# Performance work log

Hardware: AMD Instinct MI355X
Metric: run time of the kernel (lower is better)

## Reference

```python
import jax, jax.numpy as jnp
import numpy as np

EPS = 1e-6

def _ln(x, w, b):
    mu = jnp.mean(x, axis=-1, keepdims=True)
    var = jnp.mean((x - mu) ** 2, axis=-1, keepdims=True)
    return (x - mu) * jax.lax.rsqrt(var + EPS) * w + b

def setup_inputs() -> dict:
    B, N, C, H, P = 64, 197, 768, 12, 20
    Dh = C // H
    Dff = 4 * C
    key = jax.random.key(0)
    ks = jax.random.split(key, 16)
    s = 0.02
    return {
        "x": jax.random.normal(ks[0], (B, N, C), jnp.float32),
        "prompt": jax.random.normal(ks[1], (B, P, 2, H, Dh), jnp.float32),
        "ln1_w": jnp.ones((C,), jnp.float32),
        "ln1_b": jnp.zeros((C,), jnp.float32),
        "qkv_w": jax.random.normal(ks[2], (3 * C, C), jnp.float32) * s,
        "qkv_b": jnp.zeros((3 * C,), jnp.float32),
        "proj_w": jax.random.normal(ks[3], (C, C), jnp.float32) * s,
        "proj_b": jnp.zeros((C,), jnp.float32),
        "ln2_w": jnp.ones((C,), jnp.float32),
        "ln2_b": jnp.zeros((C,), jnp.float32),
        "fc1_w": jax.random.normal(ks[4], (Dff, C), jnp.float32) * s,
        "fc1_b": jnp.zeros((Dff,), jnp.float32),
        "fc2_w": jax.random.normal(ks[5], (C, Dff), jnp.float32) * s,
        "fc2_b": jnp.zeros((C,), jnp.float32),
    }

def reference(x, prompt, ln1_w, ln1_b, qkv_w, qkv_b, proj_w, proj_b,
              ln2_w, ln2_b, fc1_w, fc1_b, fc2_w, fc2_b):
    B, N, C = x.shape
    H = 12
    Dh = C // H
    scale = Dh ** -0.5

    # --- attention branch ---
    h = _ln(x, ln1_w, ln1_b)
    qkv = (h @ qkv_w.T + qkv_b).reshape(B, N, 3, H, Dh)
    qkv = jnp.transpose(qkv, (2, 0, 3, 1, 4))  # [3, B, H, N, Dh]
    q, k, v = qkv[0], qkv[1], qkv[2]

    # prompt: [B, P, 2, H, Dh] -> [2, B, H, P, Dh]
    pr = jnp.transpose(prompt, (2, 0, 3, 1, 4))
    k = jnp.concatenate([pr[0], k], axis=2)  # [B, H, P+N, Dh]
    v = jnp.concatenate([pr[1], v], axis=2)

    attn = jnp.einsum('bhnd,bhmd->bhnm', q, k) * scale
    attn = jax.nn.softmax(attn, axis=-1)
    o = jnp.einsum('bhnm,bhmd->bhnd', attn, v)
    o = jnp.transpose(o, (0, 2, 1, 3)).reshape(B, N, C)
    o = o @ proj_w.T + proj_b
    x = x + o

    # --- mlp branch ---
    h2 = _ln(x, ln2_w, ln2_b)
    m = jax.nn.gelu(h2 @ fc1_w.T + fc1_b, approximate=False)
    m = m @ fc2_w.T + fc2_b
    return x + m
```

## Files before the change

### kernel.cpp

```cpp
#include <hip/hip_runtime.h>
#include <hip/hip_bf16.h>

typedef __attribute__((ext_vector_type(4))) float f32x4;
typedef __attribute__((ext_vector_type(8))) __bf16 bfv8;
typedef __attribute__((ext_vector_type(8))) short sv8;
typedef __attribute__((ext_vector_type(4))) unsigned short usv4;


static __device__ __forceinline__ f32x4 mfma16(sv8 a, sv8 b, f32x4 c) {
    return __builtin_amdgcn_mfma_f32_16x16x32_bf16(
        __builtin_bit_cast(bfv8, a), __builtin_bit_cast(bfv8, b), c, 0, 0, 0);
}

static __device__ __forceinline__ unsigned short f2bf(float f) {
    union { float f; unsigned int u; } v; v.f = f;
    unsigned int u = v.u;
    return (unsigned short)((u + 0x7FFFu + ((u >> 16) & 1u)) >> 16);
}

static __device__ __forceinline__ void gld16(void* lds, const void* g) {
    __builtin_amdgcn_global_load_lds(
        (const __attribute__((address_space(1))) unsigned int*)g,
        (__attribute__((address_space(3))) unsigned int*)lds, 16, 0, 0);
}


__global__ void cvt_bf16_kernel(const float* __restrict__ in,
                                unsigned short* __restrict__ out, int n4) {
    int i = blockIdx.x * 256 + threadIdx.x;
    if (i >= n4) return;
    float4 f = reinterpret_cast<const float4*>(in)[i];
    usv4 o = { f2bf(f.x), f2bf(f.y), f2bf(f.z), f2bf(f.w) };
    reinterpret_cast<usv4*>(out)[i] = o;
}


__global__ void ln_kernel(const float* __restrict__ x, const float* __restrict__ w,
                          const float* __restrict__ b, unsigned short* __restrict__ out) {
    const int row = blockIdx.x;
    const int t = threadIdx.x;
    const float* xr = x + (size_t)row * 768;
    float v[3];
    float s = 0.f, ss = 0.f;
#pragma unroll
    for (int i = 0; i < 3; ++i) {
        v[i] = xr[t + i * 256];
        s += v[i]; ss += v[i] * v[i];
    }
#pragma unroll
    for (int o = 32; o; o >>= 1) { s += __shfl_xor(s, o); ss += __shfl_xor(ss, o); }
    __shared__ float red[8];
    if ((t & 63) == 0) { red[t >> 6] = s; red[4 + (t >> 6)] = ss; }
    __syncthreads();
    float S = red[0] + red[1] + red[2] + red[3];
    float SS = red[4] + red[5] + red[6] + red[7];
    float mu = S * (1.0f / 768.0f);
    float var = SS * (1.0f / 768.0f) - mu * mu;
    float rstd = rsqrtf(var + 1e-6f);
#pragma unroll
    for (int i = 0; i < 3; ++i) {
        int c = t + i * 256;
        out[(size_t)row * 768 + c] = f2bf((v[i] - mu) * rstd * w[c] + b[c]);
    }
}


__global__ void prompt_kernel(const float* __restrict__ pr,
                              unsigned short* __restrict__ k_out,
                              unsigned short* __restrict__ v_out) {
    int i = blockIdx.x * 256 + threadIdx.x;
    if (i >= 64 * 20 * 12 * 64) return;
    int d = i & 63;
    int t = i >> 6;
    int h = t % 12;
    int t2 = t / 12;
    int p = t2 % 20;
    int b = t2 / 20;
    size_t src = ((((size_t)b * 20 + p) * 2 + 0) * 12 + h) * 64 + d;
    float kv = pr[src];
    float vv = pr[src + 12 * 64];
    k_out[(((size_t)(b * 12 + h) * 224 + p) << 6) + d] = f2bf(kv);
    v_out[((size_t)(b * 12 + h) * 64 + d) * 224 + p] = f2bf(vv);
}


#define EPI_QKV 0
#define EPI_RES 1
#define EPI_GELU 2

template <int EPI, int WM, int WN>
__global__ void __launch_bounds__(WM * WN * 64)
gemm_bf16(const unsigned short* __restrict__ A,
          const unsigned short* __restrict__ W,
          const float* __restrict__ bias,
          const float* __restrict__ resid,
          void* __restrict__ out0,
          unsigned short* __restrict__ q_out,
          unsigned short* __restrict__ k_out,
          unsigned short* __restrict__ v_out,
          int M, int N, int K, int NB) {
    constexpr int THREADS = WM * WN * 64;
    constexpr int BM = WM * 64, BN = WN * 64;
    constexpr int NCA = (BM * 4) / THREADS;
    constexpr int NCB = (BN * 4) / THREADS;
    __shared__ __align__(16) unsigned short As[2][BM * 32];
    __shared__ __align__(16) unsigned short Bs[2][BN * 32];
    const int tid = threadIdx.x;
    const int lane = tid & 63;
    const int wv = tid >> 6;
    const int wm = wv / WN, wn = wv % WN;
    const int rl = lane & 15, kg = lane >> 4;

    const int nwg = gridDim.x;
    const int orig = blockIdx.x;
    const int xcd = orig & 7;
    const int qq = nwg >> 3, rr = nwg & 7;
    const int wg = (xcd < rr ? xcd * (qq + 1) : rr * (qq + 1) + (xcd - rr) * qq) + (orig >> 3);
    const int bm = wg / NB, bn = wg - bm * NB;

    const unsigned short* pA[NCA];
    const unsigned short* pB[NCB];
#pragma unroll
    for (int i = 0; i < NCA; ++i) {
        const int c = i * THREADS + tid;
        const int row = c >> 2, sl = c & 3;
        int ar = bm * BM + row; ar = ar < M ? ar : M - 1;
        pA[i] = A + (size_t)ar * K + sl * 8;
    }
#pragma unroll
    for (int i = 0; i < NCB; ++i) {
        const int c = i * THREADS + tid;
        const int row = c >> 2, sl = c & 3;
        pB[i] = W + (size_t)(bn * BN + row) * K + sl * 8;
    }
    auto stage = [&](int sb, int kt) {
        const int k0 = kt << 5;
#pragma unroll
        for (int i = 0; i < NCA; ++i)
            gld16(&As[sb][(i * THREADS + tid) * 8], pA[i] + k0);
#pragma unroll
        for (int i = 0; i < NCB; ++i)
            gld16(&Bs[sb][(i * THREADS + tid) * 8], pB[i] + k0);
    };

    f32x4 acc[4][4];
#pragma unroll
    for (int i = 0; i < 4; ++i)
#pragma unroll
        for (int j = 0; j < 4; ++j) acc[i][j] = f32x4{0.f, 0.f, 0.f, 0.f};

    const int nk = K >> 5;
    stage(0, 0);
    __syncthreads();
    for (int kt = 0; kt < nk; ++kt) {
        const int cur = kt & 1;
        if (kt + 1 < nk) stage(cur ^ 1, kt + 1);
        sv8 af[4], bfr[4];
#pragma unroll
        for (int f = 0; f < 4; ++f) {
            const int ra = wm * 64 + f * 16 + rl;
            af[f] = *reinterpret_cast<const sv8*>(&As[cur][ra * 32 + kg * 8]);
            const int rb = wn * 64 + f * 16 + rl;
            bfr[f] = *reinterpret_cast<const sv8*>(&Bs[cur][rb * 32 + kg * 8]);
        }
#pragma unroll
        for (int i = 0; i < 4; ++i)
#pragma unroll
            for (int j = 0; j < 4; ++j) acc[i][j] = mfma16(af[i], bfr[j], acc[i][j]);
        __syncthreads();
    }

#pragma unroll
    for (int i = 0; i < 4; ++i) {
        const int m0 = bm * BM + wm * 64 + i * 16 + kg * 4;
#pragma unroll
        for (int j = 0; j < 4; ++j) {
            const int ncol = bn * BN + wn * 64 + j * 16 + rl;
            const float bia = bias[ncol];
#pragma unroll
            for (int r = 0; r < 4; ++r) {
                const int m = m0 + r;
                if (m >= M) continue;
                float vv = acc[i][j][r] + bia;
                if constexpr (EPI == EPI_QKV) {
                    int b = m / 197, nn = m - b * 197;
                    int which = ncol / 768;
                    int rc = ncol - which * 768;
                    int h = rc >> 6;
                    int d = ncol & 63;
                    if (which == 0)
                        q_out[(((size_t)(b * 12 + h) * 197 + nn) << 6) + d] = f2bf(vv);
                    else if (which == 1)
                        k_out[(((size_t)(b * 12 + h) * 224 + 20 + nn) << 6) + d] = f2bf(vv);
                    else
                        v_out[((size_t)(b * 12 + h) * 64 + d) * 224 + 20 + nn] = f2bf(vv);
                } else if constexpr (EPI == EPI_RES) {
                    ((float*)out0)[(size_t)m * N + ncol] = vv + resid[(size_t)m * N + ncol];
                } else {
                    float g = vv / (1.0f + __expf(-1.5957691216f * vv * (1.0f + 0.044715f * vv * vv)));
                    ((unsigned short*)out0)[(size_t)m * N + ncol] = f2bf(g);
                }
            }
        }
    }
}


__global__ void attn_kernel(const unsigned short* __restrict__ Qg,
                            const unsigned short* __restrict__ Kg,
                            const unsigned short* __restrict__ Vtg,
                            unsigned short* __restrict__ obuf) {
    __shared__ __align__(16) unsigned short sKS[14848];
    __shared__ __align__(16) unsigned short sV[64 * 232];
    const int tid = threadIdx.x;
    const int lane = tid & 63;
    const int wave = tid >> 6;
    const int rl = lane & 15, kg = lane >> 4;
    const int qt = blockIdx.x, h = blockIdx.y, b = blockIdx.z;
    const size_t bh = (size_t)b * 12 + h;
    const size_t qbase = bh * 197 * 64;
    const size_t kbase = bh * 224 * 64;
    const size_t vbase = bh * 64 * 224;

    int qrow = qt * 64 + wave * 16 + rl;
    if (qrow > 196) qrow = 196;
    sv8 qf[2];
#pragma unroll
    for (int ks = 0; ks < 2; ++ks)
        qf[ks] = *reinterpret_cast<const sv8*>(&Qg[qbase + (size_t)qrow * 64 + ks * 32 + kg * 8]);

#pragma unroll
    for (int i = 0; i < 7; ++i) {
        const int c = i * 256 + tid;
        const int key = c >> 3, sl = c & 7;
        const int ssl = sl ^ (key & 7);
        gld16(&sKS[c * 8], &Kg[kbase + key * 64 + ssl * 8]);
    }
#pragma unroll
    for (int i = 0; i < 7; ++i) {
        const int c = i * 256 + tid;
        const int d = c / 28, sl = c - d * 28;
        sv8 val = *reinterpret_cast<const sv8*>(&Vtg[vbase + d * 224 + sl * 8]);
        *reinterpret_cast<sv8*>(&sV[d * 232 + sl * 8]) = val;
    }
    __syncthreads();

    f32x4 sacc[14];
#pragma unroll
    for (int f = 0; f < 14; ++f) sacc[f] = f32x4{0.f, 0.f, 0.f, 0.f};
#pragma unroll
    for (int f = 0; f < 14; ++f) {
        const int key = f * 16 + rl;
#pragma unroll
        for (int ks = 0; ks < 2; ++ks) {
            const int sl = (ks * 4 + kg) ^ (key & 7);
            sv8 kf = *reinterpret_cast<const sv8*>(&sKS[key * 64 + sl * 8]);
            sacc[f] = mfma16(qf[ks], kf, sacc[f]);
        }
    }

    float mx[4] = {-1e30f, -1e30f, -1e30f, -1e30f};
#pragma unroll
    for (int f = 0; f < 14; ++f) {
        const int col = f * 16 + rl;
#pragma unroll
        for (int r = 0; r < 4; ++r) {
            float s = sacc[f][r] * 0.125f;
            if (col >= 217) s = -1e30f;
            sacc[f][r] = s;
            mx[r] = fmaxf(mx[r], s);
        }
    }
#pragma unroll
    for (int o = 1; o < 16; o <<= 1)
#pragma unroll
        for (int r = 0; r < 4; ++r) mx[r] = fmaxf(mx[r], __shfl_xor(mx[r], o));
    float sm[4] = {0.f, 0.f, 0.f, 0.f};
#pragma unroll
    for (int f = 0; f < 14; ++f)
#pragma unroll
        for (int r = 0; r < 4; ++r) {
            float e = __expf(sacc[f][r] - mx[r]);
            sacc[f][r] = e;
            sm[r] += e;
        }
#pragma unroll
    for (int o = 1; o < 16; o <<= 1)
#pragma unroll
        for (int r = 0; r < 4; ++r) sm[r] += __shfl_xor(sm[r], o);
    float inv[4];
#pragma unroll
    for (int r = 0; r < 4; ++r) inv[r] = 1.0f / sm[r];

    __syncthreads();
    unsigned short* Sl = sKS;
#pragma unroll
    for (int f = 0; f < 14; ++f)
#pragma unroll
        for (int r = 0; r < 4; ++r)
            Sl[(wave * 16 + kg * 4 + r) * 232 + f * 16 + rl] = f2bf(sacc[f][r] * inv[r]);
    __syncthreads();

    f32x4 oacc[4];
#pragma unroll
    for (int fd = 0; fd < 4; ++fd) oacc[fd] = f32x4{0.f, 0.f, 0.f, 0.f};
#pragma unroll
    for (int ks = 0; ks < 7; ++ks) {
        sv8 pf = *reinterpret_cast<const sv8*>(&Sl[(wave * 16 + rl) * 232 + ks * 32 + kg * 8]);
#pragma unroll
        for (int fd = 0; fd < 4; ++fd) {
            sv8 vf = *reinterpret_cast<const sv8*>(&sV[(fd * 16 + rl) * 232 + ks * 32 + kg * 8]);
            oacc[fd] = mfma16(pf, vf, oacc[fd]);
        }
    }

#pragma unroll
    for (int fd = 0; fd < 4; ++fd)
#pragma unroll
        for (int r = 0; r < 4; ++r) {
            const int q = qt * 64 + wave * 16 + kg * 4 + r;
            if (q < 197)
                obuf[((size_t)b * 197 + q) * 768 + h * 64 + fd * 16 + rl] = f2bf(oacc[fd][r]);
        }
}


extern "C" void kernel_launch(void* const* d_in, const int* in_sizes, int n_in,
                              void* d_out, int out_size, void* d_ws, size_t ws_size,
                              hipStream_t stream) {
    const float* x      = (const float*)d_in[0];
    const float* prompt = (const float*)d_in[1];
    const float* ln1_w  = (const float*)d_in[2];
    const float* ln1_b  = (const float*)d_in[3];
    const float* qkv_w  = (const float*)d_in[4];
    const float* qkv_b  = (const float*)d_in[5];
    const float* proj_w = (const float*)d_in[6];
    const float* proj_b = (const float*)d_in[7];
    const float* ln2_w  = (const float*)d_in[8];
    const float* ln2_b  = (const float*)d_in[9];
    const float* fc1_w  = (const float*)d_in[10];
    const float* fc1_b  = (const float*)d_in[11];
    const float* fc2_w  = (const float*)d_in[12];
    const float* fc2_b  = (const float*)d_in[13];

    char* ws = (char*)d_ws;
    size_t off = 0;
    auto bump = [&](size_t bytes) {
        char* p = ws + off;
        off += (bytes + 255) & ~(size_t)255;
        return p;
    };
    unsigned short* qkvw  = (unsigned short*)bump(2304UL * 768 * 2);
    unsigned short* projw = (unsigned short*)bump(768UL * 768 * 2);
    unsigned short* fc1w  = (unsigned short*)bump(3072UL * 768 * 2);
    unsigned short* fc2w  = (unsigned short*)bump(768UL * 3072 * 2);
    unsigned short* h2    = (unsigned short*)bump(12608UL * 768 * 2);
    float* xmid           = (float*)bump(12608UL * 768 * 4);
    char* pool = ws + off;
    unsigned short* h1   = (unsigned short*)(pool);
    unsigned short* Qg   = (unsigned short*)(pool + 19365888UL);
    unsigned short* Kg   = (unsigned short*)(pool + 38731776UL);
    unsigned short* Vtg  = (unsigned short*)(pool + 60751872UL);
    unsigned short* obuf = (unsigned short*)(pool + 82771968UL);
    unsigned short* mbuf = (unsigned short*)(pool);

    cvt_bf16_kernel<<<(2304 * 768 / 4 + 255) / 256, 256, 0, stream>>>(qkv_w, qkvw, 2304 * 768 / 4);
    cvt_bf16_kernel<<<(768 * 768 / 4 + 255) / 256, 256, 0, stream>>>(proj_w, projw, 768 * 768 / 4);
    cvt_bf16_kernel<<<(3072 * 768 / 4 + 255) / 256, 256, 0, stream>>>(fc1_w, fc1w, 3072 * 768 / 4);
    cvt_bf16_kernel<<<(768 * 3072 / 4 + 255) / 256, 256, 0, stream>>>(fc2_w, fc2w, 768 * 3072 / 4);

    ln_kernel<<<12608, 256, 0, stream>>>(x, ln1_w, ln1_b, h1);
    prompt_kernel<<<983040 / 256, 256, 0, stream>>>(prompt, Kg, Vtg);

    gemm_bf16<EPI_QKV, 4, 4><<<50 * 9, 1024, 0, stream>>>(
        h1, qkvw, qkv_b, nullptr, nullptr, Qg, Kg, Vtg, 12608, 2304, 768, 9);

    attn_kernel<<<dim3(4, 12, 64), 256, 0, stream>>>(Qg, Kg, Vtg, obuf);

    gemm_bf16<EPI_RES, 2, 2><<<99 * 6, 256, 0, stream>>>(
        obuf, projw, proj_b, x, xmid, nullptr, nullptr, nullptr, 12608, 768, 768, 6);

    ln_kernel<<<12608, 256, 0, stream>>>(xmid, ln2_w, ln2_b, h2);

    gemm_bf16<EPI_GELU, 4, 4><<<50 * 12, 1024, 0, stream>>>(
        h2, fc1w, fc1_b, nullptr, mbuf, nullptr, nullptr, nullptr, 12608, 3072, 768, 12);

    gemm_bf16<EPI_RES, 2, 2><<<99 * 6, 256, 0, stream>>>(
        mbuf, fc2w, fc2_b, xmid, (float*)d_out, nullptr, nullptr, nullptr, 12608, 768, 3072, 6);
}
```

Before: 444.2 us.

## Fuse weight conversion, prompt packing and LN1 into one prep kernel; retile GEMMs

Merges the four weight-conversion launches, the prompt K/V packing kernel and the first LayerNorm into a single block-dispatched prep kernel. LayerNorm now reads and writes float4 vectors using 192 active threads per row. The QKV and FC1 GEMMs move from 256x256 tiles with 1024 threads to 256x128 tiles with 512 threads, doubling the grid. The aim is lower launch overhead and better CU occupancy on the large GEMMs, at the cost of more A-tile reloads.

```diff
diff --git a/kernel.cpp b/kernel.cpp
--- a/kernel.cpp
+++ b/kernel.cpp
@@ -25,157 +25,103 @@
 }
 
 
-__global__ void cvt_bf16_kernel(const float* __restrict__ in,
-                                unsigned short* __restrict__ out, int n4) {
-    int i = blockIdx.x * 256 + threadIdx.x;
-    if (i >= n4) return;
-    float4 f = reinterpret_cast<const float4*>(in)[i];
-    usv4 o = { f2bf(f.x), f2bf(f.y), f2bf(f.z), f2bf(f.w) };
-    reinterpret_cast<usv4*>(out)[i] = o;
-}
-
+static __device__ __forceinline__ void ln_row(const float* __restrict__ xr,
+                                              const float* __restrict__ w,
+                                              const float* __restrict__ b,
+                                              unsigned short* __restrict__ outr,
+                                              int t) {
+    __shared__ float red[8];
+    float4 v = {0.f, 0.f, 0.f, 0.f};
+    float s = 0.f, ss = 0.f;
+    if (t < 192) {
+        v = reinterpret_cast<const float4*>(xr)[t];
+        s = v.x + v.y + v.z + v.w;
+        ss = v.x * v.x + v.y * v.y + v.z * v.z + v.w * v.w;
+    }
+#pragma unroll
+    for (int o = 32; o; o >>= 1) { s += __shfl_xor(s, o); ss += __shfl_xor(ss, o); }
+    if ((t & 63) == 0) { red[t >> 6] = s; red[4 + (t >> 6)] = ss; }
+    __syncthreads();
+    const float S = red[0] + red[1] + red[2];
+    const float SS = red[4] + red[5] + red[6];
+    const float mu = S * (1.0f / 768.0f);
+    const float var = SS * (1.0f / 768.0f) - mu * mu;
+    const float rstd = rsqrtf(var + 1e-6f);
+    if (t < 192) {
+        float4 wv = reinterpret_cast<const float4*>(w)[t];
+        float4 bv = reinterpret_cast<const float4*>(b)[t];
+        usv4 o = { f2bf((v.x - mu) * rstd * wv.x + bv.x),
+                   f2bf((v.y - mu) * rstd * wv.y + bv.y),
+                   f2bf((v.z - mu) * rstd * wv.z + bv.z),
+                   f2bf((v.w - mu) * rstd * wv.w + bv.w) };
+        reinterpret_cast<usv4*>(outr)[t] = o;
+    }
+}
 
 __global__ void ln_kernel(const float* __restrict__ x, const float* __restrict__ w,
                           const float* __restrict__ b, unsigned short* __restrict__ out) {
-    const int row = blockIdx.x;
-    const int t = threadIdx.x;
-    const float* xr = x + (size_t)row * 768;
-    float v[3];
-    float s = 0.f, ss = 0.f;
-#pragma unroll
-    for (int i = 0; i < 3; ++i) {
-        v[i] = xr[t + i * 256];
-        s += v[i]; ss += v[i] * v[i];
-    }
-#pragma unroll
-    for (int o = 32; o; o >>= 1) { s += __shfl_xor(s, o); ss += __shfl_xor(ss, o); }
-    __shared__ float red[8];
-    if ((t & 63) == 0) { red[t >> 6] = s; red[4 + (t >> 6)] = ss; }
-    __syncthreads();
-    float S = red[0] + red[1] + red[2] + red[3];
-    float SS = red[4] + red[5] + red[6] + red[7];
-    float mu = S * (1.0f / 768.0f);
-    float var = SS * (1.0f / 768.0f) - mu * mu;
-    float rstd = rsqrtf(var + 1e-6f);
-#pragma unroll
-    for (int i = 0; i < 3; ++i) {
-        int c = t + i * 256;
-        out[(size_t)row * 768 + c] = f2bf((v[i] - mu) * rstd * w[c] + b[c]);
-    }
-}
-
-
-__global__ void prompt_kernel(const float* __restrict__ pr,
-                              unsigned short* __restrict__ k_out,
-                              unsigned short* __restrict__ v_out) {
-    int i = blockIdx.x * 256 + threadIdx.x;
-    if (i >= 64 * 20 * 12 * 64) return;
-    int d = i & 63;
-    int t = i >> 6;
-    int h = t % 12;
-    int t2 = t / 12;
-    int p = t2 % 20;
-    int b = t2 / 20;
-    size_t src = ((((size_t)b * 20 + p) * 2 + 0) * 12 + h) * 64 + d;
-    float kv = pr[src];
-    float vv = pr[src + 12 * 64];
-    k_out[(((size_t)(b * 12 + h) * 224 + p) << 6) + d] = f2bf(kv);
-    v_out[((size_t)(b * 12 + h) * 64 + d) * 224 + p] = f2bf(vv);
-}
-
+    const size_t row = blockIdx.x;
+    ln_row(x + row * 768, w, b, out + row * 768, threadIdx.x);
+}
+
+
+__global__ void prep_kernel(const float* __restrict__ qkv_w, const float* __restrict__ proj_w,
+                            const float* __restrict__ fc1_w, const float* __restrict__ fc2_w,
+                            unsigned short* __restrict__ qkvw, unsigned short* __restrict__ projw,
+                            unsigned short* __restrict__ fc1w, unsigned short* __restrict__ fc2w,
+                            const float* __restrict__ pr,
+                            unsigned short* __restrict__ k_out, unsigned short* __restrict__ v_out,
+                            const float* __restrict__ x, const float* __restrict__ ln1_w,
+                            const float* __restrict__ ln1_b, unsigned short* __restrict__ h1) {
+    const int blk = blockIdx.x;
+    const int tid = threadIdx.x;
+    if (blk < 6912) {
+        const float* in;
+        unsigned short* out;
+        int i;
+        if (blk < 1728)      { in = qkv_w; out = qkvw; i = blk * 256 + tid; }
+        else if (blk < 2304) { in = proj_w; out = projw; i = (blk - 1728) * 256 + tid; }
+        else if (blk < 4608) { in = fc1_w; out = fc1w; i = (blk - 2304) * 256 + tid; }
+        else                 { in = fc2_w; out = fc2w; i = (blk - 4608) * 256 + tid; }
+        float4 f = reinterpret_cast<const float4*>(in)[i];
+        usv4 o = { f2bf(f.x), f2bf(f.y), f2bf(f.z), f2bf(f.w) };
+        reinterpret_cast<usv4*>(out)[i] = o;
+    } else if (blk < 10752) {
+        const int i = (blk - 6912) * 256 + tid;
+        const int d = i & 63;
+        const int t = i >> 6;
+        const int h = t % 12;
+        const int t2 = t / 12;
+        const int p = t2 % 20;
+        const int b = t2 / 20;
+        size_t src = ((((size_t)b * 20 + p) * 2 + 0) * 12 + h) * 64 + d;
+        float kv = pr[src];
+        float vv = pr[src + 12 * 64];
+        k_out[(((size_t)(b * 12 + h) * 224 + p) << 6) + d] = f2bf(kv);
+        v_out[((size_t)(b * 12 + h) * 64 + d) * 224 + p] = f2bf(vv);
+    } else {
+        const size_t row = blk - 10752;
+        ln_row(x + row * 768, ln1_w, ln1_b, h1 + row * 768, tid);
+    }
+}
 
 #define EPI_QKV 0
 #define EPI_RES 1
 #define EPI_GELU 2
 
-template <int EPI, int WM, int WN>
-__global__ void __launch_bounds__(WM * WN * 64)
-gemm_bf16(const unsigned short* __restrict__ A,
-          const unsigned short* __restrict__ W,
-          const float* __restrict__ bias,
-          const float* __restrict__ resid,
-          void* __restrict__ out0,
-          unsigned short* __restrict__ q_out,
-          unsigned short* __restrict__ k_out,
-          unsigned short* __restrict__ v_out,
-          int M, int N, int K, int NB) {
-    constexpr int THREADS = WM * WN * 64;
-    constexpr int BM = WM * 64, BN = WN * 64;
-    constexpr int NCA = (BM * 4) / THREADS;
-    constexpr int NCB = (BN * 4) / THREADS;
-    __shared__ __align__(16) unsigned short As[2][BM * 32];
-    __shared__ __align__(16) unsigned short Bs[2][BN * 32];
-    const int tid = threadIdx.x;
-    const int lane = tid & 63;
-    const int wv = tid >> 6;
-    const int wm = wv / WN, wn = wv % WN;
-    const int rl = lane & 15, kg = lane >> 4;
-
-    const int nwg = gridDim.x;
-    const int orig = blockIdx.x;
-    const int xcd = orig & 7;
-    const int qq = nwg >> 3, rr = nwg & 7;
-    const int wg = (xcd < rr ? xcd * (qq + 1) : rr * (qq + 1) + (xcd - rr) * qq) + (orig >> 3);
-    const int bm = wg / NB, bn = wg - bm * NB;
-
-    const unsigned short* pA[NCA];
-    const unsigned short* pB[NCB];
-#pragma unroll
-    for (int i = 0; i < NCA; ++i) {
-        const int c = i * THREADS + tid;
-        const int row = c >> 2, sl = c & 3;
-        int ar = bm * BM + row; ar = ar < M ? ar : M - 1;
-        pA[i] = A + (size_t)ar * K + sl * 8;
-    }
-#pragma unroll
-    for (int i = 0; i < NCB; ++i) {
-        const int c = i * THREADS + tid;
-        const int row = c >> 2, sl = c & 3;
-        pB[i] = W + (size_t)(bn * BN + row) * K + sl * 8;
-    }
-    auto stage = [&](int sb, int kt) {
-        const int k0 = kt << 5;
-#pragma unroll
-        for (int i = 0; i < NCA; ++i)
-            gld16(&As[sb][(i * THREADS + tid) * 8], pA[i] + k0);
-#pragma unroll
-        for (int i = 0; i < NCB; ++i)
-            gld16(&Bs[sb][(i * THREADS + tid) * 8], pB[i] + k0);
-    };
-
-    f32x4 acc[4][4];
-#pragma unroll
-    for (int i = 0; i < 4; ++i)
-#pragma unroll
-        for (int j = 0; j < 4; ++j) acc[i][j] = f32x4{0.f, 0.f, 0.f, 0.f};
-
-    const int nk = K >> 5;
-    stage(0, 0);
-    __syncthreads();
-    for (int kt = 0; kt < nk; ++kt) {
-        const int cur = kt & 1;
-        if (kt + 1 < nk) stage(cur ^ 1, kt + 1);
-        sv8 af[4], bfr[4];
-#pragma unroll
-        for (int f = 0; f < 4; ++f) {
-            const int ra = wm * 64 + f * 16 + rl;
-            af[f] = *reinterpret_cast<const sv8*>(&As[cur][ra * 32 + kg * 8]);
-            const int rb = wn * 64 + f * 16 + rl;
-            bfr[f] = *reinterpret_cast<const sv8*>(&Bs[cur][rb * 32 + kg * 8]);
-        }
-#pragma unroll
-        for (int i = 0; i < 4; ++i)
-#pragma unroll
-            for (int j = 0; j < 4; ++j) acc[i][j] = mfma16(af[i], bfr[j], acc[i][j]);
-        __syncthreads();
-    }
-
+
+template <int EPI>
+static __device__ __forceinline__ void gemm_epilogue(
+        f32x4 (&acc)[4][4], int bmBase, int bnBase, int wm, int wn,
+        int rl, int kg, const float* bias, const float* resid, void* out0,
+        unsigned short* q_out, unsigned short* k_out, unsigned short* v_out,
+        int M, int N) {
 #pragma unroll
     for (int i = 0; i < 4; ++i) {
-        const int m0 = bm * BM + wm * 64 + i * 16 + kg * 4;
+        const int m0 = bmBase + wm * 64 + i * 16 + kg * 4;
 #pragma unroll
         for (int j = 0; j < 4; ++j) {
-            const int ncol = bn * BN + wn * 64 + j * 16 + rl;
+            const int ncol = bnBase + wn * 64 + j * 16 + rl;
             const float bia = bias[ncol];
 #pragma unroll
             for (int r = 0; r < 4; ++r) {
@@ -206,6 +152,92 @@
 }
 
 
+template <int EPI, int WM, int WN>
+__global__ void __launch_bounds__(WM * WN * 64)
+gemm_bf16(const unsigned short* __restrict__ A,
+          const unsigned short* __restrict__ W,
+          const float* __restrict__ bias,
+          const float* __restrict__ resid,
+          void* __restrict__ out0,
+          unsigned short* __restrict__ q_out,
+          unsigned short* __restrict__ k_out,
+          unsigned short* __restrict__ v_out,
+          int M, int N, int K, int NB) {
+    constexpr int THREADS = WM * WN * 64;
+    constexpr int BM = WM * 64, BN = WN * 64;
+    constexpr int NCA = (BM * 4) / THREADS;
+    constexpr int NCB = (BN * 4) / THREADS;
+    __shared__ __align__(16) unsigned short As[2][BM * 32];
+    __shared__ __align__(16) unsigned short Bs[2][BN * 32];
+    const int tid = threadIdx.x;
+    const int lane = tid & 63;
+    const int wv = tid >> 6;
+    const int wm = wv / WN, wn = wv % WN;
+    const int rl = lane & 15, kg = lane >> 4;
+
+    const int nwg = gridDim.x;
+    const int orig = blockIdx.x;
+    const int xcd = orig & 7;
+    const int qq = nwg >> 3, rr = nwg & 7;
+    const int wg = (xcd < rr ? xcd * (qq + 1) : rr * (qq + 1) + (xcd - rr) * qq) + (orig >> 3);
+    const int bm = wg / NB, bn = wg - bm * NB;
+
+    const unsigned short* pA[NCA];
+    const unsigned short* pB[NCB];
+#pragma unroll
+    for (int i = 0; i < NCA; ++i) {
+        const int c = i * THREADS + tid;
+        const int row = c >> 2, sl = c & 3;
+        int ar = bm * BM + row; ar = ar < M ? ar : M - 1;
+        pA[i] = A + (size_t)ar * K + sl * 8;
+    }
+#pragma unroll
+    for (int i = 0; i < NCB; ++i) {
+        const int c = i * THREADS + tid;
+        const int row = c >> 2, sl = c & 3;
+        pB[i] = W + (size_t)(bn * BN + row) * K + sl * 8;
+    }
+    auto stage = [&](int sb, int kt) {
+        const int k0 = kt << 5;
+#pragma unroll
+        for (int i = 0; i < NCA; ++i)
+            gld16(&As[sb][(i * THREADS + tid) * 8], pA[i] + k0);
+#pragma unroll
+        for (int i = 0; i < NCB; ++i)
+            gld16(&Bs[sb][(i * THREADS + tid) * 8], pB[i] + k0);
+    };
+
+    f32x4 acc[4][4];
+#pragma unroll
+    for (int i = 0; i < 4; ++i)
+#pragma unroll
+        for (int j = 0; j < 4; ++j) acc[i][j] = f32x4{0.f, 0.f, 0.f, 0.f};
+
+    const int nk = K >> 5;
+    stage(0, 0);
+    __syncthreads();
+    for (int kt = 0; kt < nk; ++kt) {
+        const int cur = kt & 1;
+        if (kt + 1 < nk) stage(cur ^ 1, kt + 1);
+        sv8 af[4], bfr[4];
+#pragma unroll
+        for (int f = 0; f < 4; ++f) {
+            const int ra = wm * 64 + f * 16 + rl;
+            af[f] = *reinterpret_cast<const sv8*>(&As[cur][ra * 32 + kg * 8]);
+            const int rb = wn * 64 + f * 16 + rl;
+            bfr[f] = *reinterpret_cast<const sv8*>(&Bs[cur][rb * 32 + kg * 8]);
+        }
+#pragma unroll
+        for (int i = 0; i < 4; ++i)
+#pragma unroll
+            for (int j = 0; j < 4; ++j) acc[i][j] = mfma16(af[i], bfr[j], acc[i][j]);
+        __syncthreads();
+    }
+    gemm_epilogue<EPI>(acc, bm * BM, bn * BN, wm, wn, rl, kg, bias, resid,
+                       out0, q_out, k_out, v_out, M, N);
+}
+
+
 __global__ void attn_kernel(const unsigned short* __restrict__ Qg,
                             const unsigned short* __restrict__ Kg,
                             const unsigned short* __restrict__ Vtg,
@@ -364,16 +396,12 @@
     unsigned short* obuf = (unsigned short*)(pool + 82771968UL);
     unsigned short* mbuf = (unsigned short*)(pool);
 
-    cvt_bf16_kernel<<<(2304 * 768 / 4 + 255) / 256, 256, 0, stream>>>(qkv_w, qkvw, 2304 * 768 / 4);
-    cvt_bf16_kernel<<<(768 * 768 / 4 + 255) / 256, 256, 0, stream>>>(proj_w, projw, 768 * 768 / 4);
-    cvt_bf16_kernel<<<(3072 * 768 / 4 + 255) / 256, 256, 0, stream>>>(fc1_w, fc1w, 3072 * 768 / 4);
-    cvt_bf16_kernel<<<(768 * 3072 / 4 + 255) / 256, 256, 0, stream>>>(fc2_w, fc2w, 768 * 3072 / 4);
-
-    ln_kernel<<<12608, 256, 0, stream>>>(x, ln1_w, ln1_b, h1);
-    prompt_kernel<<<983040 / 256, 256, 0, stream>>>(prompt, Kg, Vtg);
-
-    gemm_bf16<EPI_QKV, 4, 4><<<50 * 9, 1024, 0, stream>>>(
-        h1, qkvw, qkv_b, nullptr, nullptr, Qg, Kg, Vtg, 12608, 2304, 768, 9);
+    prep_kernel<<<23360, 256, 0, stream>>>(
+        qkv_w, proj_w, fc1_w, fc2_w, qkvw, projw, fc1w, fc2w,
+        prompt, Kg, Vtg, x, ln1_w, ln1_b, h1);
+
+    gemm_bf16<EPI_QKV, 4, 2><<<50 * 18, 512, 0, stream>>>(
+        h1, qkvw, qkv_b, nullptr, nullptr, Qg, Kg, Vtg, 12608, 2304, 768, 18);
 
     attn_kernel<<<dim3(4, 12, 64), 256, 0, stream>>>(Qg, Kg, Vtg, obuf);
 
@@ -382,8 +410,8 @@
 
     ln_kernel<<<12608, 256, 0, stream>>>(xmid, ln2_w, ln2_b, h2);
 
-    gemm_bf16<EPI_GELU, 4, 4><<<50 * 12, 1024, 0, stream>>>(
-        h2, fc1w, fc1_b, nullptr, mbuf, nullptr, nullptr, nullptr, 12608, 3072, 768, 12);
+    gemm_bf16<EPI_GELU, 4, 2><<<50 * 24, 512, 0, stream>>>(
+        h2, fc1w, fc1_b, nullptr, mbuf, nullptr, nullptr, nullptr, 12608, 3072, 768, 24);
 
     gemm_bf16<EPI_RES, 2, 2><<<99 * 6, 256, 0, stream>>>(
         mbuf, fc2w, fc2_b, xmid, (float*)d_out, nullptr, nullptr, nullptr, 12608, 768, 3072, 6);
```

After: 410.6 us. 1.08x faster.
